# Kernel tuning notes

Hardware: AMD Instinct MI355X
Metric: run time of the kernel (lower is better)

The kernel has to match this reference:

```python
import jax, jax.numpy as jnp
import numpy as np

E = 1024
H = 16
D = E // H
S = 2048
B = 2

def setup_inputs() -> dict:
    key = jax.random.key(0)
    ks = jax.random.split(key, 5)
    x = jax.random.normal(ks[0], (B, S, E), dtype=jnp.float32)
    W_qkv = jax.random.normal(ks[1], (E, 3 * E), dtype=jnp.float32) / np.sqrt(E)
    b_qkv = jax.random.normal(ks[2], (3 * E,), dtype=jnp.float32) * 0.02
    W_out = jax.random.normal(ks[3], (E, E), dtype=jnp.float32) / np.sqrt(E)
    b_out = jax.random.normal(ks[4], (E,), dtype=jnp.float32) * 0.02
    return {"x": x, "W_qkv": W_qkv, "b_qkv": b_qkv, "W_out": W_out, "b_out": b_out}

def reference(x, W_qkv, b_qkv, W_out, b_out):
    b, s, e = x.shape
    qkv = x @ W_qkv + b_qkv                      # [B,S,3E]
    q, k, v = jnp.split(qkv, 3, axis=-1)
    # [B,S,E] -> [B,H,S,D]
    q = q.reshape(b, s, H, D).transpose(0, 2, 1, 3)
    k = k.reshape(b, s, H, D).transpose(0, 2, 1, 3)
    v = v.reshape(b, s, H, D).transpose(0, 2, 1, 3)
    scale = 1.0 / np.sqrt(D)
    att = jnp.einsum('bhqd,bhkd->bhqk', q, k) * scale
    causal = jnp.tril(jnp.ones((s, s), dtype=bool))
    att = jnp.where(causal[None, None], att, -jnp.inf)
    att = jax.nn.softmax(att, axis=-1)
    out = jnp.einsum('bhqk,bhkd->bhqd', att, v)  # [B,H,S,D]
    out = out.transpose(0, 2, 1, 3).reshape(b, s, e)
    return out @ W_out + b_out
```

## Files before the change

### kernel.cpp

```cpp
#include <hip/hip_runtime.h>

typedef unsigned short u16;
typedef __bf16  bf16x8 __attribute__((ext_vector_type(8)));
typedef float   f32x4  __attribute__((ext_vector_type(4)));
typedef unsigned int   u32x4 __attribute__((ext_vector_type(4)));
typedef unsigned short u16x4 __attribute__((ext_vector_type(4)));
typedef unsigned short u16x8 __attribute__((ext_vector_type(8)));

#define BB 2
#define HH 16
#define DD 64
#define SS 2048
#define EE 1024

#define QSCALE 0.1803368801111244f

static __device__ __forceinline__ u16 f2bf(float f) {
    unsigned int u = __float_as_uint(f);
    u += 0x7FFFu + ((u >> 16) & 1u);
    return (u16)(u >> 16);
}

union BfCast { u32x4 u; bf16x8 b; };
static __device__ __forceinline__ bf16x8 ldb8(const u16* p) {
    BfCast x; x.u = *(const u32x4*)p; return x.b;
}

static __device__ __forceinline__ void gload16(const u16* g, u16* l) {
    __builtin_amdgcn_global_load_lds(
        (const __attribute__((address_space(1))) unsigned int*)g,
        (__attribute__((address_space(3))) unsigned int*)l, 16, 0, 0);
}

#define UG (32 * 512)
static __device__ __forceinline__ int kidx(int s, int d) {
    return (((s >> 4) * 2 + (d >> 5)) * 512) + ((((d >> 3) & 3) * 16 + (s & 15)) * 8) + (d & 7);
}
static __device__ __forceinline__ int vidx(int key, int d) {
    return (((key >> 5) * 4 + (d >> 4)) * 512) + ((((key >> 3) & 3) * 16 + (d & 15)) * 8) + (key & 7);
}

__global__ __launch_bounds__(256) void prep_kernel(
    const float* __restrict__ x,    u16* __restrict__ xb,
    const float* __restrict__ Wqkv, u16* __restrict__ wqkvT,
    const float* __restrict__ Wout, u16* __restrict__ woutT)
{
    __shared__ float tile[32][33];
    const int bid = blockIdx.x;
    if (bid < 2048) {
        const int t = bid * 256 + threadIdx.x;
        const int u = t >> 6, w = t & 63;
        const int m = (u >> 5) * 16 + (w & 15);
        const int k = (u & 31) * 32 + (w >> 4) * 8;
        const float* p = x + m * 1024 + k;
        const f32x4 a = *(const f32x4*)p;
        const f32x4 b = *(const f32x4*)(p + 4);
        u16x8 o;
        o[0] = f2bf(a[0]); o[1] = f2bf(a[1]); o[2] = f2bf(a[2]); o[3] = f2bf(a[3]);
        o[4] = f2bf(b[0]); o[5] = f2bf(b[1]); o[6] = f2bf(b[2]); o[7] = f2bf(b[3]);
        *(u16x8*)&xb[u * 512 + w * 8] = o;
        return;
    }
    const float* in; u16* out; int C, tb;
    if (bid < 2048 + 3072) { in = Wqkv; out = wqkvT; C = 3072; tb = bid - 2048; }
    else                   { in = Wout; out = woutT; C = 1024; tb = bid - 5120; }
    const int tx = threadIdx.x & 31;
    const int ty = threadIdx.x >> 5;
    const int ct = C >> 5;
    const int bc = tb % ct, br = tb / ct;
    const int c0 = bc * 32, r0 = br * 32;
    #pragma unroll
    for (int i = 0; i < 4; i++)
        tile[ty + i * 8][tx] = in[(r0 + ty + i * 8) * C + c0 + tx];
    __syncthreads();
    #pragma unroll
    for (int i = 0; i < 4; i++) {
        const int n = c0 + ty + i * 8;
        out[((n >> 4) * 32 + (r0 >> 5)) * 512 + (((tx >> 3) & 3) * 16 + (n & 15)) * 8 + (tx & 7)]
            = f2bf(tile[tx][ty + i * 8]);
    }
}

__global__ __launch_bounds__(256, 3) void gemm_qkv_kernel(
    const u16* __restrict__ Af,
    const u16* __restrict__ Bf,
    const float* __restrict__ bias,
    u16* __restrict__ Qb, u16* __restrict__ Kb, u16* __restrict__ Vb)
{
    __shared__ __align__(16) u16 Bs[2][8 * 512];
    const int lane = threadIdx.x & 63;
    const int wave = threadIdx.x >> 6;
    const int nb = 3 * EE / 128;
    const int tm = blockIdx.x / nb, tn = blockIdx.x % nb;
    const int lm = lane & 15, quad = lane >> 4;
    const int wy = wave >> 1, wx = wave & 1;

    const u16* bg = Bf + (tn * 8 + 2 * wave) * UG + lane * 8;
    u16* bl0 = &Bs[0][2 * wave * 512];
    u16* bl1 = &Bs[1][2 * wave * 512];
    const u16* ag[4];
    #pragma unroll
    for (int i = 0; i < 4; i++)
        ag[i] = Af + (tm * 8 + wy * 4 + i) * UG + lane * 8;

    f32x4 acc[4][4] = {};
    bf16x8 a0[4], a1[4];

    gload16(bg,      bl0);
    gload16(bg + UG, bl0 + 512);
    #pragma unroll
    for (int i = 0; i < 4; i++) a0[i] = ldb8(ag[i]);

    #pragma unroll 1
    for (int it = 0; it < 32; it += 2) {
        __syncthreads();
        if (it + 1 < 32) {
            gload16(bg + (it + 1) * 512,      bl1);
            gload16(bg + UG + (it + 1) * 512, bl1 + 512);
            #pragma unroll
            for (int i = 0; i < 4; i++) a1[i] = ldb8(ag[i] + (it + 1) * 512);
        }
        {
            bf16x8 bf[4];
            #pragma unroll
            for (int i = 0; i < 4; i++)
                bf[i] = ldb8(&Bs[0][(wx * 4 + i) * 512 + lane * 8]);
            #pragma unroll
            for (int mi = 0; mi < 4; mi++)
                #pragma unroll
                for (int ni = 0; ni < 4; ni++)
                    acc[mi][ni] = __builtin_amdgcn_mfma_f32_16x16x32_bf16(a0[mi], bf[ni], acc[mi][ni], 0, 0, 0);
        }
        __syncthreads();
        if (it + 2 < 32) {
            gload16(bg + (it + 2) * 512,      bl0);
            gload16(bg + UG + (it + 2) * 512, bl0 + 512);
            #pragma unroll
            for (int i = 0; i < 4; i++) a0[i] = ldb8(ag[i] + (it + 2) * 512);
        }
        {
            bf16x8 bf[4];
            #pragma unroll
            for (int i = 0; i < 4; i++)
                bf[i] = ldb8(&Bs[1][(wx * 4 + i) * 512 + lane * 8]);
            #pragma unroll
            for (int mi = 0; mi < 4; mi++)
                #pragma unroll
                for (int ni = 0; ni < 4; ni++)
                    acc[mi][ni] = __builtin_amdgcn_mfma_f32_16x16x32_bf16(a1[mi], bf[ni], acc[mi][ni], 0, 0, 0);
        }
    }

    const int gm0 = tm * 128 + wy * 64;
    const int gn0 = tn * 128 + wx * 64;
    #pragma unroll
    for (int ni = 0; ni < 4; ni++) {
        const int n = gn0 + ni * 16 + lm;
        const float bv = bias[n];
        const int which = n >> 10;
        const int e = n & 1023;
        const int h = e >> 6, d = e & 63;
        #pragma unroll
        for (int mi = 0; mi < 4; mi++) {
            if (which == 2) {
                const int m0 = gm0 + mi * 16 + quad * 4;
                const int b = m0 >> 11, key0 = m0 & 2047;
                u16x4 pk;
                #pragma unroll
                for (int r = 0; r < 4; r++) pk[r] = f2bf(acc[mi][ni][r] + bv);
                *(u16x4*)&Vb[(b * HH + h) * 131072 + vidx(key0, d)] = pk;
            } else if (which == 1) {
                #pragma unroll
                for (int r = 0; r < 4; r++) {
                    const int m = gm0 + mi * 16 + quad * 4 + r;
                    const int b = m >> 11, s = m & 2047;
                    Kb[(b * HH + h) * 131072 + kidx(s, d)] = f2bf(acc[mi][ni][r] + bv);
                }
            } else {
                #pragma unroll
                for (int r = 0; r < 4; r++) {
                    const int m = gm0 + mi * 16 + quad * 4 + r;
                    const int b = m >> 11, s = m & 2047;
                    Qb[((b * HH + h) * SS + s) * DD + d] = f2bf((acc[mi][ni][r] + bv) * QSCALE);
                }
            }
        }
    }
}

__global__ __launch_bounds__(256) void attn_kernel(
    const u16* __restrict__ Qb, const u16* __restrict__ Kb,
    const u16* __restrict__ Vb, u16* __restrict__ Ob)
{
    __shared__ __align__(16) u16 Ks[2][4096];
    __shared__ __align__(16) u16 Vs[2][4096];
    __shared__ __align__(16) u16 Plds[4 * 16 * 72];
    const int tid = threadIdx.x;
    const int lane = tid & 63, wave = tid >> 6;
    const int lm = lane & 15, quad = lane >> 4;
    const int bh = blockIdx.x & 31;
    const int qt = (SS / 64 - 1) - (blockIdx.x >> 5);
    const int q0 = qt * 64;
    const int qrow = q0 + wave * 16;
    const int b = bh >> 4, h = bh & 15;

    const u16* qbase = Qb + (bh * SS + qrow) * DD;
    const bf16x8 qf0 = ldb8(qbase + lm * DD + quad * 8);
    const bf16x8 qf1 = ldb8(qbase + lm * DD + 32 + quad * 8);

    const u16* ktile = Kb + bh * 131072;
    const u16* vtile = Vb + bh * 131072;
    u16* Pw = Plds + wave * (16 * 72);

    BfCast oc; oc.u = (u32x4){0x3F803F80u, 0x3F803F80u, 0x3F803F80u, 0x3F803F80u};
    const bf16x8 ones = oc.b;

    f32x4 oacc[4] = {};
    f32x4 lacc = {0.f, 0.f, 0.f, 0.f};

    const int ktmax = qt + 1;
    {
        const u16* kg = ktile + wave * 1024 + lane * 8;
        const u16* vg = vtile + wave * 1024 + lane * 8;
        gload16(kg,       &Ks[0][wave * 1024]);
        gload16(kg + 512, &Ks[0][wave * 1024 + 512]);
        gload16(vg,       &Vs[0][wave * 1024]);
        gload16(vg + 512, &Vs[0][wave * 1024 + 512]);
    }
    for (int kt = 0; kt < ktmax; ++kt) {
        const int cur = kt & 1;
        const int k0 = kt * 64;
        __syncthreads();
        if (kt + 1 < ktmax) {
            const u16* kg = ktile + (kt + 1) * 4096 + wave * 1024 + lane * 8;
            const u16* vg = vtile + (kt + 1) * 4096 + wave * 1024 + lane * 8;
            gload16(kg,       &Ks[cur ^ 1][wave * 1024]);
            gload16(kg + 512, &Ks[cur ^ 1][wave * 1024 + 512]);
            gload16(vg,       &Vs[cur ^ 1][wave * 1024]);
            gload16(vg + 512, &Vs[cur ^ 1][wave * 1024 + 512]);
        }

        f32x4 s[4];
        #pragma unroll
        for (int g = 0; g < 4; g++) {
            f32x4 z = {0.f, 0.f, 0.f, 0.f};
            z    = __builtin_amdgcn_mfma_f32_16x16x32_bf16(ldb8(&Ks[cur][(g * 2) * 512 + lane * 8]), qf0, z, 0, 0, 0);
            s[g] = __builtin_amdgcn_mfma_f32_16x16x32_bf16(ldb8(&Ks[cur][(g * 2 + 1) * 512 + lane * 8]), qf1, z, 0, 0, 0);
        }
        if (k0 + 63 > qrow) {
            const int lim = qrow + lm - k0 - quad * 4;
            #pragma unroll
            for (int g = 0; g < 4; g++)
                #pragma unroll
                for (int r = 0; r < 4; r++)
                    if (g * 16 + r > lim) s[g][r] = -INFINITY;
        }
        #pragma unroll
        for (int g = 0; g < 4; g++) {
            u16x4 pk;
            #pragma unroll
            for (int r = 0; r < 4; r++) pk[r] = f2bf(__builtin_amdgcn_exp2f(s[g][r]));
            *(u16x4*)&Pw[lm * 72 + g * 16 + quad * 4] = pk;
        }
        const bf16x8 pf0 = ldb8(&Pw[lm * 72 + quad * 8]);
        const bf16x8 pf1 = ldb8(&Pw[lm * 72 + 32 + quad * 8]);
        lacc = __builtin_amdgcn_mfma_f32_16x16x32_bf16(ones, pf0, lacc, 0, 0, 0);
        lacc = __builtin_amdgcn_mfma_f32_16x16x32_bf16(ones, pf1, lacc, 0, 0, 0);
        #pragma unroll
        for (int dg = 0; dg < 4; dg++) {
            oacc[dg] = __builtin_amdgcn_mfma_f32_16x16x32_bf16(ldb8(&Vs[cur][dg * 512 + lane * 8]), pf0, oacc[dg], 0, 0, 0);
            oacc[dg] = __builtin_amdgcn_mfma_f32_16x16x32_bf16(ldb8(&Vs[cur][(4 + dg) * 512 + lane * 8]), pf1, oacc[dg], 0, 0, 0);
        }
    }
    const float inv = 1.0f / lacc[0];
    u16* ob = Ob + (((b * SS + qrow) >> 4) * 32 + h * 2) * 512;
    #pragma unroll
    for (int dg = 0; dg < 4; dg++) {
        u16x4 pk;
        #pragma unroll
        for (int r = 0; r < 4; r++) pk[r] = f2bf(oacc[dg][r] * inv);
        *(u16x4*)&ob[(dg >> 1) * 512 + (((dg * 2 + (quad >> 1)) & 3) * 16 + lm) * 8 + (quad & 1) * 4] = pk;
    }
}

__global__ __launch_bounds__(256) void gemm_out_kernel(
    const u16* __restrict__ Af,
    const u16* __restrict__ Bf,
    const float* __restrict__ bias,
    float* __restrict__ Out)
{
    __shared__ __align__(16) u16 Bs[2][8 * 512];
    const int lane = threadIdx.x & 63;
    const int wave = threadIdx.x >> 6;
    const int nb = EE / 128;
    const int tm = blockIdx.x / nb, tn = blockIdx.x % nb;
    const int lm = lane & 15, quad = lane >> 4;
    const int wy = wave >> 1, wx = wave & 1;

    const u16* bg = Bf + (tn * 8 + 2 * wave) * UG + lane * 8;
    u16* bl0 = &Bs[0][2 * wave * 512];
    u16* bl1 = &Bs[1][2 * wave * 512];
    const u16* ag[2];
    #pragma unroll
    for (int i = 0; i < 2; i++)
        ag[i] = Af + (tm * 4 + wy * 2 + i) * UG + lane * 8;

    f32x4 acc[2][4] = {};
    bf16x8 a0[2], a1[2];

    gload16(bg,      bl0);
    gload16(bg + UG, bl0 + 512);
    #pragma unroll
    for (int i = 0; i < 2; i++) a0[i] = ldb8(ag[i]);

    #pragma unroll 1
    for (int it = 0; it < 32; it += 2) {
        __syncthreads();
        if (it + 1 < 32) {
            gload16(bg + (it + 1) * 512,      bl1);
            gload16(bg + UG + (it + 1) * 512, bl1 + 512);
            #pragma unroll
            for (int i = 0; i < 2; i++) a1[i] = ldb8(ag[i] + (it + 1) * 512);
        }
        {
            bf16x8 bf[4];
            #pragma unroll
            for (int i = 0; i < 4; i++)
                bf[i] = ldb8(&Bs[0][(wx * 4 + i) * 512 + lane * 8]);
            #pragma unroll
            for (int mi = 0; mi < 2; mi++)
                #pragma unroll
                for (int ni = 0; ni < 4; ni++)
                    acc[mi][ni] = __builtin_amdgcn_mfma_f32_16x16x32_bf16(a0[mi], bf[ni], acc[mi][ni], 0, 0, 0);
        }
        __syncthreads();
        if (it + 2 < 32) {
            gload16(bg + (it + 2) * 512,      bl0);
            gload16(bg + UG + (it + 2) * 512, bl0 + 512);
            #pragma unroll
            for (int i = 0; i < 2; i++) a0[i] = ldb8(ag[i] + (it + 2) * 512);
        }
        {
            bf16x8 bf[4];
            #pragma unroll
            for (int i = 0; i < 4; i++)
                bf[i] = ldb8(&Bs[1][(wx * 4 + i) * 512 + lane * 8]);
            #pragma unroll
            for (int mi = 0; mi < 2; mi++)
                #pragma unroll
                for (int ni = 0; ni < 4; ni++)
                    acc[mi][ni] = __builtin_amdgcn_mfma_f32_16x16x32_bf16(a1[mi], bf[ni], acc[mi][ni], 0, 0, 0);
        }
    }

    const int gm0 = tm * 64 + wy * 32;
    const int gn0 = tn * 128 + wx * 64;
    #pragma unroll
    for (int ni = 0; ni < 4; ni++) {
        const int n = gn0 + ni * 16 + lm;
        const float bv = bias[n];
        #pragma unroll
        for (int mi = 0; mi < 2; mi++)
            #pragma unroll
            for (int r = 0; r < 4; r++)
                Out[(gm0 + mi * 16 + quad * 4 + r) * EE + n] = acc[mi][ni][r] + bv;
    }
}

extern "C" void kernel_launch(void* const* d_in, const int* in_sizes, int n_in,
                              void* d_out, int out_size, void* d_ws, size_t ws_size,
                              hipStream_t stream)
{
    const float* x     = (const float*)d_in[0];
    const float* Wqkv  = (const float*)d_in[1];
    const float* bqkv  = (const float*)d_in[2];
    const float* Wout  = (const float*)d_in[3];
    const float* bout  = (const float*)d_in[4];
    float* out = (float*)d_out;

    char* ws = (char*)d_ws;
    u16* xb    = (u16*)(ws + 0);
    u16* wqkvT = (u16*)(ws + 8388608);
    u16* woutT = (u16*)(ws + 14680064);
    u16* Qb    = (u16*)(ws + 16777216);
    u16* Kb    = (u16*)(ws + 25165824);
    u16* Vb    = (u16*)(ws + 33554432);
    u16* Ob    = (u16*)(ws + 41943040);
    if (ws_size < 50331648) return;

    prep_kernel<<<2048 + 3072 + 1024, 256, 0, stream>>>(x, xb, Wqkv, wqkvT, Wout, woutT);
    gemm_qkv_kernel<<<(BB * SS / 128) * (3 * EE / 128), 256, 0, stream>>>(xb, wqkvT, bqkv, Qb, Kb, Vb);
    attn_kernel<<<BB * HH * (SS / 64), 256, 0, stream>>>(Qb, Kb, Vb, Ob);
    gemm_out_kernel<<<(BB * SS / 64) * (EE / 128), 256, 0, stream>>>(Ob, woutT, bout, out);
}
```

Before: 174.8 us.

## Fuse all four stages into one persistent kernel with grid barriers

Replaces the four launches (prep, QKV GEMM, attention, output GEMM) with a single persistent kernel of 512 blocks. Stages are separated by atomic-counter grid barriers, and the GEMM and attention stages pull work items from atomic tile counters. The goal is to remove launch gaps and tail effects between kernels. In exchange it adds a hipMemsetAsync, spin-wait barriers that depend on all 512 blocks being co-resident (the spin has a guard that breaks out after a fixed count, which could let a block proceed before the others finish), and forces launch_bounds(256,3) on the attention stage.

```diff
diff --git a/kernel.cpp b/kernel.cpp
--- a/kernel.cpp
+++ b/kernel.cpp
@@ -40,15 +40,39 @@
     return (((key >> 5) * 4 + (d >> 4)) * 512) + ((((key >> 3) & 3) * 16 + (d & 15)) * 8) + (key & 7);
 }
 
-__global__ __launch_bounds__(256) void prep_kernel(
+static __device__ __forceinline__ void gbar(unsigned int* bar, unsigned int target) {
+    __syncthreads();
+    if (threadIdx.x == 0) {
+        __threadfence();
+        atomicAdd(bar, 1u);
+        unsigned int guard = 0;
+        while (atomicAdd(bar, 0u) < target) {
+            if (++guard > (1u << 22)) break;
+        }
+        __threadfence();
+    }
+    __syncthreads();
+}
+
+__global__ __launch_bounds__(256, 3) void fused_kernel(
     const float* __restrict__ x,    u16* __restrict__ xb,
     const float* __restrict__ Wqkv, u16* __restrict__ wqkvT,
-    const float* __restrict__ Wout, u16* __restrict__ woutT)
+    const float* __restrict__ Wout, u16* __restrict__ woutT,
+    const float* __restrict__ bqkv,
+    u16* __restrict__ Qb, u16* __restrict__ Kb, u16* __restrict__ Vb,
+    u16* __restrict__ Ob,
+    const float* __restrict__ bout, float* __restrict__ Out,
+    unsigned int* __restrict__ cnt)
 {
-    __shared__ float tile[32][33];
+    __shared__ __align__(16) u16 smem[21120];
+    __shared__ unsigned int su;
     const int bid = blockIdx.x;
-    if (bid < 2048) {
-        const int t = bid * 256 + threadIdx.x;
+    const int tid = threadIdx.x;
+    const int lane = tid & 63, wave = tid >> 6;
+    const int lm = lane & 15, quad = lane >> 4;
+
+    for (int cb = bid; cb < 2048; cb += 512) {
+        const int t = cb * 256 + tid;
         const int u = t >> 6, w = t & 63;
         const int m = (u >> 5) * 16 + (w & 15);
         const int k = (u & 31) * 32 + (w >> 4) * 8;
@@ -59,311 +83,307 @@
         o[0] = f2bf(a[0]); o[1] = f2bf(a[1]); o[2] = f2bf(a[2]); o[3] = f2bf(a[3]);
         o[4] = f2bf(b[0]); o[5] = f2bf(b[1]); o[6] = f2bf(b[2]); o[7] = f2bf(b[3]);
         *(u16x8*)&xb[u * 512 + w * 8] = o;
-        return;
-    }
-    const float* in; u16* out; int C, tb;
-    if (bid < 2048 + 3072) { in = Wqkv; out = wqkvT; C = 3072; tb = bid - 2048; }
-    else                   { in = Wout; out = woutT; C = 1024; tb = bid - 5120; }
-    const int tx = threadIdx.x & 31;
-    const int ty = threadIdx.x >> 5;
-    const int ct = C >> 5;
-    const int bc = tb % ct, br = tb / ct;
-    const int c0 = bc * 32, r0 = br * 32;
-    #pragma unroll
-    for (int i = 0; i < 4; i++)
-        tile[ty + i * 8][tx] = in[(r0 + ty + i * 8) * C + c0 + tx];
-    __syncthreads();
-    #pragma unroll
-    for (int i = 0; i < 4; i++) {
-        const int n = c0 + ty + i * 8;
-        out[((n >> 4) * 32 + (r0 >> 5)) * 512 + (((tx >> 3) & 3) * 16 + (n & 15)) * 8 + (tx & 7)]
-            = f2bf(tile[tx][ty + i * 8]);
-    }
-}
-
-__global__ __launch_bounds__(256, 3) void gemm_qkv_kernel(
-    const u16* __restrict__ Af,
-    const u16* __restrict__ Bf,
-    const float* __restrict__ bias,
-    u16* __restrict__ Qb, u16* __restrict__ Kb, u16* __restrict__ Vb)
-{
-    __shared__ __align__(16) u16 Bs[2][8 * 512];
-    const int lane = threadIdx.x & 63;
-    const int wave = threadIdx.x >> 6;
-    const int nb = 3 * EE / 128;
-    const int tm = blockIdx.x / nb, tn = blockIdx.x % nb;
-    const int lm = lane & 15, quad = lane >> 4;
-    const int wy = wave >> 1, wx = wave & 1;
-
-    const u16* bg = Bf + (tn * 8 + 2 * wave) * UG + lane * 8;
-    u16* bl0 = &Bs[0][2 * wave * 512];
-    u16* bl1 = &Bs[1][2 * wave * 512];
-    const u16* ag[4];
-    #pragma unroll
-    for (int i = 0; i < 4; i++)
-        ag[i] = Af + (tm * 8 + wy * 4 + i) * UG + lane * 8;
-
-    f32x4 acc[4][4] = {};
-    bf16x8 a0[4], a1[4];
-
-    gload16(bg,      bl0);
-    gload16(bg + UG, bl0 + 512);
-    #pragma unroll
-    for (int i = 0; i < 4; i++) a0[i] = ldb8(ag[i]);
-
-    #pragma unroll 1
-    for (int it = 0; it < 32; it += 2) {
-        __syncthreads();
-        if (it + 1 < 32) {
-            gload16(bg + (it + 1) * 512,      bl1);
-            gload16(bg + UG + (it + 1) * 512, bl1 + 512);
-            #pragma unroll
-            for (int i = 0; i < 4; i++) a1[i] = ldb8(ag[i] + (it + 1) * 512);
-        }
-        {
-            bf16x8 bf[4];
+    }
+    {
+        float* tile = (float*)smem;
+        const int tx = tid & 31, ty = tid >> 5;
+        for (int tb = bid; tb < 4096; tb += 512) {
+            const float* in; u16* out; int C, b2;
+            if (tb < 3072) { in = Wqkv; out = wqkvT; C = 3072; b2 = tb; }
+            else           { in = Wout; out = woutT; C = 1024; b2 = tb - 3072; }
+            const int ct = C >> 5;
+            const int bc = b2 % ct, br = b2 / ct;
+            const int c0 = bc * 32, r0 = br * 32;
+            __syncthreads();
             #pragma unroll
             for (int i = 0; i < 4; i++)
-                bf[i] = ldb8(&Bs[0][(wx * 4 + i) * 512 + lane * 8]);
+                tile[(ty + i * 8) * 33 + tx] = in[(r0 + ty + i * 8) * C + c0 + tx];
+            __syncthreads();
             #pragma unroll
-            for (int mi = 0; mi < 4; mi++)
-                #pragma unroll
-                for (int ni = 0; ni < 4; ni++)
-                    acc[mi][ni] = __builtin_amdgcn_mfma_f32_16x16x32_bf16(a0[mi], bf[ni], acc[mi][ni], 0, 0, 0);
-        }
-        __syncthreads();
-        if (it + 2 < 32) {
-            gload16(bg + (it + 2) * 512,      bl0);
-            gload16(bg + UG + (it + 2) * 512, bl0 + 512);
+            for (int i = 0; i < 4; i++) {
+                const int n = c0 + ty + i * 8;
+                out[((n >> 4) * 32 + (r0 >> 5)) * 512 + (((tx >> 3) & 3) * 16 + (n & 15)) * 8 + (tx & 7)]
+                    = f2bf(tile[tx * 33 + ty + i * 8]);
+            }
+        }
+    }
+    gbar(cnt, 512);
+
+    {
+        const int wy = wave >> 1, wx = wave & 1;
+        for (;;) {
+            __syncthreads();
+            if (tid == 0) su = atomicAdd(cnt + 16, 1u);
+            __syncthreads();
+            const int uq = (int)su;
+            if (uq >= 768) break;
+            const int tm = uq / 24, tn = uq % 24;
+
+            const u16* bg = wqkvT + (tn * 8 + 2 * wave) * UG + lane * 8;
+            u16* bl0 = smem + 2 * wave * 512;
+            u16* bl1 = smem + 4096 + 2 * wave * 512;
+            const u16* ag0 = xb + (tm * 8 + wy * 4 + 0) * UG + lane * 8;
+            const u16* ag1 = xb + (tm * 8 + wy * 4 + 1) * UG + lane * 8;
+            const u16* ag2 = xb + (tm * 8 + wy * 4 + 2) * UG + lane * 8;
+            const u16* ag3 = xb + (tm * 8 + wy * 4 + 3) * UG + lane * 8;
+
+            f32x4 acc[4][4] = {};
+            bf16x8 a0[4], a1[4];
+
+            gload16(bg,      bl0);
+            gload16(bg + UG, bl0 + 512);
+            a0[0] = ldb8(ag0); a0[1] = ldb8(ag1); a0[2] = ldb8(ag2); a0[3] = ldb8(ag3);
+
+            #pragma unroll 1
+            for (int it = 0; it < 32; it += 2) {
+                __syncthreads();
+                if (it + 1 < 32) {
+                    gload16(bg + (it + 1) * 512,      bl1);
+                    gload16(bg + UG + (it + 1) * 512, bl1 + 512);
+                    a1[0] = ldb8(ag0 + (it + 1) * 512);
+                    a1[1] = ldb8(ag1 + (it + 1) * 512);
+                    a1[2] = ldb8(ag2 + (it + 1) * 512);
+                    a1[3] = ldb8(ag3 + (it + 1) * 512);
+                }
+                {
+                    bf16x8 bf[4];
+                    #pragma unroll
+                    for (int i = 0; i < 4; i++)
+                        bf[i] = ldb8(smem + (wx * 4 + i) * 512 + lane * 8);
+                    #pragma unroll
+                    for (int mi = 0; mi < 4; mi++)
+                        #pragma unroll
+                        for (int ni = 0; ni < 4; ni++)
+                            acc[mi][ni] = __builtin_amdgcn_mfma_f32_16x16x32_bf16(a0[mi], bf[ni], acc[mi][ni], 0, 0, 0);
+                }
+                __syncthreads();
+                if (it + 2 < 32) {
+                    gload16(bg + (it + 2) * 512,      bl0);
+                    gload16(bg + UG + (it + 2) * 512, bl0 + 512);
+                    a0[0] = ldb8(ag0 + (it + 2) * 512);
+                    a0[1] = ldb8(ag1 + (it + 2) * 512);
+                    a0[2] = ldb8(ag2 + (it + 2) * 512);
+                    a0[3] = ldb8(ag3 + (it + 2) * 512);
+                }
+                {
+                    bf16x8 bf[4];
+                    #pragma unroll
+                    for (int i = 0; i < 4; i++)
+                        bf[i] = ldb8(smem + 4096 + (wx * 4 + i) * 512 + lane * 8);
+                    #pragma unroll
+                    for (int mi = 0; mi < 4; mi++)
+                        #pragma unroll
+                        for (int ni = 0; ni < 4; ni++)
+                            acc[mi][ni] = __builtin_amdgcn_mfma_f32_16x16x32_bf16(a1[mi], bf[ni], acc[mi][ni], 0, 0, 0);
+                }
+            }
+
+            const int gm0 = tm * 128 + wy * 64;
+            const int gn0 = tn * 128 + wx * 64;
             #pragma unroll
-            for (int i = 0; i < 4; i++) a0[i] = ldb8(ag[i] + (it + 2) * 512);
-        }
-        {
-            bf16x8 bf[4];
+            for (int ni = 0; ni < 4; ni++) {
+                const int n = gn0 + ni * 16 + lm;
+                const float bv = bqkv[n];
+                const int which = n >> 10;
+                const int e = n & 1023;
+                const int h = e >> 6, d = e & 63;
+                #pragma unroll
+                for (int mi = 0; mi < 4; mi++) {
+                    if (which == 2) {
+                        const int m0 = gm0 + mi * 16 + quad * 4;
+                        const int b = m0 >> 11, key0 = m0 & 2047;
+                        u16x4 pk;
+                        #pragma unroll
+                        for (int r = 0; r < 4; r++) pk[r] = f2bf(acc[mi][ni][r] + bv);
+                        *(u16x4*)&Vb[(b * HH + h) * 131072 + vidx(key0, d)] = pk;
+                    } else if (which == 1) {
+                        #pragma unroll
+                        for (int r = 0; r < 4; r++) {
+                            const int m = gm0 + mi * 16 + quad * 4 + r;
+                            const int b = m >> 11, s = m & 2047;
+                            Kb[(b * HH + h) * 131072 + kidx(s, d)] = f2bf(acc[mi][ni][r] + bv);
+                        }
+                    } else {
+                        #pragma unroll
+                        for (int r = 0; r < 4; r++) {
+                            const int m = gm0 + mi * 16 + quad * 4 + r;
+                            const int b = m >> 11, s = m & 2047;
+                            Qb[((b * HH + h) * SS + s) * DD + d] = f2bf((acc[mi][ni][r] + bv) * QSCALE);
+                        }
+                    }
+                }
+            }
+        }
+    }
+    gbar(cnt, 1024);
+
+    {
+        u16* Pw = smem + 16384 + wave * (16 * 72);
+        BfCast oc; oc.u = (u32x4){0x3F803F80u, 0x3F803F80u, 0x3F803F80u, 0x3F803F80u};
+        const bf16x8 ones = oc.b;
+
+        for (;;) {
+            __syncthreads();
+            if (tid == 0) su = atomicAdd(cnt + 32, 1u);
+            __syncthreads();
+            const int u = (int)su;
+            if (u >= 1024) break;
+            const int bh = u & 31;
+            const int qt = (SS / 64 - 1) - (u >> 5);
+            const int q0 = qt * 64;
+            const int qrow = q0 + wave * 16;
+            const int b = bh >> 4, h = bh & 15;
+
+            const u16* qbase = Qb + (bh * SS + qrow) * DD;
+            const bf16x8 qf0 = ldb8(qbase + lm * DD + quad * 8);
+            const bf16x8 qf1 = ldb8(qbase + lm * DD + 32 + quad * 8);
+
+            const u16* ktile = Kb + bh * 131072;
+            const u16* vtile = Vb + bh * 131072;
+
+            f32x4 oacc[4] = {};
+            f32x4 lacc = {0.f, 0.f, 0.f, 0.f};
+
+            const int ktmax = qt + 1;
+            {
+                const u16* kg = ktile + wave * 1024 + lane * 8;
+                const u16* vg = vtile + wave * 1024 + lane * 8;
+                gload16(kg,       smem + wave * 1024);
+                gload16(kg + 512, smem + wave * 1024 + 512);
+                gload16(vg,       smem + 8192 + wave * 1024);
+                gload16(vg + 512, smem + 8192 + wave * 1024 + 512);
+            }
+            for (int kt = 0; kt < ktmax; ++kt) {
+                const int cur = kt & 1;
+                const int k0 = kt * 64;
+                u16* Kcur = smem + cur * 4096;
+                u16* Vcur = smem + 8192 + cur * 4096;
+                __syncthreads();
+                if (kt + 1 < ktmax) {
+                    u16* Knxt = smem + (cur ^ 1) * 4096;
+                    u16* Vnxt = smem + 8192 + (cur ^ 1) * 4096;
+                    const u16* kg = ktile + (kt + 1) * 4096 + wave * 1024 + lane * 8;
+                    const u16* vg = vtile + (kt + 1) * 4096 + wave * 1024 + lane * 8;
+                    gload16(kg,       Knxt + wave * 1024);
+                    gload16(kg + 512, Knxt + wave * 1024 + 512);
+                    gload16(vg,       Vnxt + wave * 1024);
+                    gload16(vg + 512, Vnxt + wave * 1024 + 512);
+                }
+
+                f32x4 s[4];
+                #pragma unroll
+                for (int g = 0; g < 4; g++) {
+                    f32x4 z = {0.f, 0.f, 0.f, 0.f};
+                    z    = __builtin_amdgcn_mfma_f32_16x16x32_bf16(ldb8(Kcur + (g * 2) * 512 + lane * 8), qf0, z, 0, 0, 0);
+                    s[g] = __builtin_amdgcn_mfma_f32_16x16x32_bf16(ldb8(Kcur + (g * 2 + 1) * 512 + lane * 8), qf1, z, 0, 0, 0);
+                }
+                if (k0 + 63 > qrow) {
+                    const int lim = qrow + lm - k0 - quad * 4;
+                    #pragma unroll
+                    for (int g = 0; g < 4; g++)
+                        #pragma unroll
+                        for (int r = 0; r < 4; r++)
+                            if (g * 16 + r > lim) s[g][r] = -INFINITY;
+                }
+                #pragma unroll
+                for (int g = 0; g < 4; g++) {
+                    u16x4 pk;
+                    #pragma unroll
+                    for (int r = 0; r < 4; r++) pk[r] = f2bf(__builtin_amdgcn_exp2f(s[g][r]));
+                    *(u16x4*)&Pw[lm * 72 + g * 16 + quad * 4] = pk;
+                }
+                const bf16x8 pf0 = ldb8(&Pw[lm * 72 + quad * 8]);
+                const bf16x8 pf1 = ldb8(&Pw[lm * 72 + 32 + quad * 8]);
+                lacc = __builtin_amdgcn_mfma_f32_16x16x32_bf16(ones, pf0, lacc, 0, 0, 0);
+                lacc = __builtin_amdgcn_mfma_f32_16x16x32_bf16(ones, pf1, lacc, 0, 0, 0);
+                #pragma unroll
+                for (int dg = 0; dg < 4; dg++) {
+                    oacc[dg] = __builtin_amdgcn_mfma_f32_16x16x32_bf16(ldb8(Vcur + dg * 512 + lane * 8), pf0, oacc[dg], 0, 0, 0);
+                    oacc[dg] = __builtin_amdgcn_mfma_f32_16x16x32_bf16(ldb8(Vcur + (4 + dg) * 512 + lane * 8), pf1, oacc[dg], 0, 0, 0);
+                }
+            }
+            const float inv = 1.0f / lacc[0];
+            u16* ob = Ob + (((b * SS + qrow) >> 4) * 32 + h * 2) * 512;
             #pragma unroll
-            for (int i = 0; i < 4; i++)
-                bf[i] = ldb8(&Bs[1][(wx * 4 + i) * 512 + lane * 8]);
-            #pragma unroll
-            for (int mi = 0; mi < 4; mi++)
-                #pragma unroll
-                for (int ni = 0; ni < 4; ni++)
-                    acc[mi][ni] = __builtin_amdgcn_mfma_f32_16x16x32_bf16(a1[mi], bf[ni], acc[mi][ni], 0, 0, 0);
-        }
-    }
-
-    const int gm0 = tm * 128 + wy * 64;
-    const int gn0 = tn * 128 + wx * 64;
-    #pragma unroll
-    for (int ni = 0; ni < 4; ni++) {
-        const int n = gn0 + ni * 16 + lm;
-        const float bv = bias[n];
-        const int which = n >> 10;
-        const int e = n & 1023;
-        const int h = e >> 6, d = e & 63;
+            for (int dg = 0; dg < 4; dg++) {
+                u16x4 pk;
+                #pragma unroll
+                for (int r = 0; r < 4; r++) pk[r] = f2bf(oacc[dg][r] * inv);
+                *(u16x4*)&ob[(dg >> 1) * 512 + (((dg * 2 + (quad >> 1)) & 3) * 16 + lm) * 8 + (quad & 1) * 4] = pk;
+            }
+        }
+    }
+    gbar(cnt, 1536);
+
+    {
+        const int tm = bid / 8, tn = bid % 8;
+        const int wy = wave >> 1, wx = wave & 1;
+
+        const u16* bg = woutT + (tn * 8 + 2 * wave) * UG + lane * 8;
+        u16* bl0 = smem + 2 * wave * 512;
+        u16* bl1 = smem + 4096 + 2 * wave * 512;
+        const u16* ag0 = Ob + (tm * 4 + wy * 2 + 0) * UG + lane * 8;
+        const u16* ag1 = Ob + (tm * 4 + wy * 2 + 1) * UG + lane * 8;
+
+        f32x4 acc[2][4] = {};
+        bf16x8 a0[2], a1[2];
+
+        gload16(bg,      bl0);
+        gload16(bg + UG, bl0 + 512);
+        a0[0] = ldb8(ag0); a0[1] = ldb8(ag1);
+
+        #pragma unroll 1
+        for (int it = 0; it < 32; it += 2) {
+            __syncthreads();
+            if (it + 1 < 32) {
+                gload16(bg + (it + 1) * 512,      bl1);
+                gload16(bg + UG + (it + 1) * 512, bl1 + 512);
+                a1[0] = ldb8(ag0 + (it + 1) * 512);
+                a1[1] = ldb8(ag1 + (it + 1) * 512);
+            }
+            {
+                bf16x8 bf[4];
+                #pragma unroll
+                for (int i = 0; i < 4; i++)
+                    bf[i] = ldb8(smem + (wx * 4 + i) * 512 + lane * 8);
+                #pragma unroll
+                for (int mi = 0; mi < 2; mi++)
+                    #pragma unroll
+                    for (int ni = 0; ni < 4; ni++)
+                        acc[mi][ni] = __builtin_amdgcn_mfma_f32_16x16x32_bf16(a0[mi], bf[ni], acc[mi][ni], 0, 0, 0);
+            }
+            __syncthreads();
+            if (it + 2 < 32) {
+                gload16(bg + (it + 2) * 512,      bl0);
+                gload16(bg + UG + (it + 2) * 512, bl0 + 512);
+                a0[0] = ldb8(ag0 + (it + 2) * 512);
+                a0[1] = ldb8(ag1 + (it + 2) * 512);
+            }
+            {
+                bf16x8 bf[4];
+                #pragma unroll
+                for (int i = 0; i < 4; i++)
+                    bf[i] = ldb8(smem + 4096 + (wx * 4 + i) * 512 + lane * 8);
+                #pragma unroll
+                for (int mi = 0; mi < 2; mi++)
+                    #pragma unroll
+                    for (int ni = 0; ni < 4; ni++)
+                        acc[mi][ni] = __builtin_amdgcn_mfma_f32_16x16x32_bf16(a1[mi], bf[ni], acc[mi][ni], 0, 0, 0);
+            }
+        }
+
+        const int gm0 = tm * 64 + wy * 32;
+        const int gn0 = tn * 128 + wx * 64;
         #pragma unroll
-        for (int mi = 0; mi < 4; mi++) {
-            if (which == 2) {
-                const int m0 = gm0 + mi * 16 + quad * 4;
-                const int b = m0 >> 11, key0 = m0 & 2047;
-                u16x4 pk;
-                #pragma unroll
-                for (int r = 0; r < 4; r++) pk[r] = f2bf(acc[mi][ni][r] + bv);
-                *(u16x4*)&Vb[(b * HH + h) * 131072 + vidx(key0, d)] = pk;
-            } else if (which == 1) {
-                #pragma unroll
-                for (int r = 0; r < 4; r++) {
-                    const int m = gm0 + mi * 16 + quad * 4 + r;
-                    const int b = m >> 11, s = m & 2047;
-                    Kb[(b * HH + h) * 131072 + kidx(s, d)] = f2bf(acc[mi][ni][r] + bv);
-                }
-            } else {
-                #pragma unroll
-                for (int r = 0; r < 4; r++) {
-                    const int m = gm0 + mi * 16 + quad * 4 + r;
-                    const int b = m >> 11, s = m & 2047;
-                    Qb[((b * HH + h) * SS + s) * DD + d] = f2bf((acc[mi][ni][r] + bv) * QSCALE);
-                }
-            }
-        }
-    }
-}
-
-__global__ __launch_bounds__(256) void attn_kernel(
-    const u16* __restrict__ Qb, const u16* __restrict__ Kb,
-    const u16* __restrict__ Vb, u16* __restrict__ Ob)
-{
-    __shared__ __align__(16) u16 Ks[2][4096];
-    __shared__ __align__(16) u16 Vs[2][4096];
-    __shared__ __align__(16) u16 Plds[4 * 16 * 72];
-    const int tid = threadIdx.x;
-    const int lane = tid & 63, wave = tid >> 6;
-    const int lm = lane & 15, quad = lane >> 4;
-    const int bh = blockIdx.x & 31;
-    const int qt = (SS / 64 - 1) - (blockIdx.x >> 5);
-    const int q0 = qt * 64;
-    const int qrow = q0 + wave * 16;
-    const int b = bh >> 4, h = bh & 15;
-
-    const u16* qbase = Qb + (bh * SS + qrow) * DD;
-    const bf16x8 qf0 = ldb8(qbase + lm * DD + quad * 8);
-    const bf16x8 qf1 = ldb8(qbase + lm * DD + 32 + quad * 8);
-
-    const u16* ktile = Kb + bh * 131072;
-    const u16* vtile = Vb + bh * 131072;
-    u16* Pw = Plds + wave * (16 * 72);
-
-    BfCast oc; oc.u = (u32x4){0x3F803F80u, 0x3F803F80u, 0x3F803F80u, 0x3F803F80u};
-    const bf16x8 ones = oc.b;
-
-    f32x4 oacc[4] = {};
-    f32x4 lacc = {0.f, 0.f, 0.f, 0.f};
-
-    const int ktmax = qt + 1;
-    {
-        const u16* kg = ktile + wave * 1024 + lane * 8;
-        const u16* vg = vtile + wave * 1024 + lane * 8;
-        gload16(kg,       &Ks[0][wave * 1024]);
-        gload16(kg + 512, &Ks[0][wave * 1024 + 512]);
-        gload16(vg,       &Vs[0][wave * 1024]);
-        gload16(vg + 512, &Vs[0][wave * 1024 + 512]);
-    }
-    for (int kt = 0; kt < ktmax; ++kt) {
-        const int cur = kt & 1;
-        const int k0 = kt * 64;
-        __syncthreads();
-        if (kt + 1 < ktmax) {
-            const u16* kg = ktile + (kt + 1) * 4096 + wave * 1024 + lane * 8;
-            const u16* vg = vtile + (kt + 1) * 4096 + wave * 1024 + lane * 8;
-            gload16(kg,       &Ks[cur ^ 1][wave * 1024]);
-            gload16(kg + 512, &Ks[cur ^ 1][wave * 1024 + 512]);
-            gload16(vg,       &Vs[cur ^ 1][wave * 1024]);
-            gload16(vg + 512, &Vs[cur ^ 1][wave * 1024 + 512]);
-        }
-
-        f32x4 s[4];
-        #pragma unroll
-        for (int g = 0; g < 4; g++) {
-            f32x4 z = {0.f, 0.f, 0.f, 0.f};
-            z    = __builtin_amdgcn_mfma_f32_16x16x32_bf16(ldb8(&Ks[cur][(g * 2) * 512 + lane * 8]), qf0, z, 0, 0, 0);
-            s[g] = __builtin_amdgcn_mfma_f32_16x16x32_bf16(ldb8(&Ks[cur][(g * 2 + 1) * 512 + lane * 8]), qf1, z, 0, 0, 0);
-        }
-        if (k0 + 63 > qrow) {
-            const int lim = qrow + lm - k0 - quad * 4;
-            #pragma unroll
-            for (int g = 0; g < 4; g++)
-                #pragma unroll
-                for (int r = 0; r < 4; r++)
-                    if (g * 16 + r > lim) s[g][r] = -INFINITY;
-        }
-        #pragma unroll
-        for (int g = 0; g < 4; g++) {
-            u16x4 pk;
-            #pragma unroll
-            for (int r = 0; r < 4; r++) pk[r] = f2bf(__builtin_amdgcn_exp2f(s[g][r]));
-            *(u16x4*)&Pw[lm * 72 + g * 16 + quad * 4] = pk;
-        }
-        const bf16x8 pf0 = ldb8(&Pw[lm * 72 + quad * 8]);
-        const bf16x8 pf1 = ldb8(&Pw[lm * 72 + 32 + quad * 8]);
-        lacc = __builtin_amdgcn_mfma_f32_16x16x32_bf16(ones, pf0, lacc, 0, 0, 0);
-        lacc = __builtin_amdgcn_mfma_f32_16x16x32_bf16(ones, pf1, lacc, 0, 0, 0);
-        #pragma unroll
-        for (int dg = 0; dg < 4; dg++) {
-            oacc[dg] = __builtin_amdgcn_mfma_f32_16x16x32_bf16(ldb8(&Vs[cur][dg * 512 + lane * 8]), pf0, oacc[dg], 0, 0, 0);
-            oacc[dg] = __builtin_amdgcn_mfma_f32_16x16x32_bf16(ldb8(&Vs[cur][(4 + dg) * 512 + lane * 8]), pf1, oacc[dg], 0, 0, 0);
-        }
-    }
-    const float inv = 1.0f / lacc[0];
-    u16* ob = Ob + (((b * SS + qrow) >> 4) * 32 + h * 2) * 512;
-    #pragma unroll
-    for (int dg = 0; dg < 4; dg++) {
-        u16x4 pk;
-        #pragma unroll
-        for (int r = 0; r < 4; r++) pk[r] = f2bf(oacc[dg][r] * inv);
-        *(u16x4*)&ob[(dg >> 1) * 512 + (((dg * 2 + (quad >> 1)) & 3) * 16 + lm) * 8 + (quad & 1) * 4] = pk;
-    }
-}
-
-__global__ __launch_bounds__(256) void gemm_out_kernel(
-    const u16* __restrict__ Af,
-    const u16* __restrict__ Bf,
-    const float* __restrict__ bias,
-    float* __restrict__ Out)
-{
-    __shared__ __align__(16) u16 Bs[2][8 * 512];
-    const int lane = threadIdx.x & 63;
-    const int wave = threadIdx.x >> 6;
-    const int nb = EE / 128;
-    const int tm = blockIdx.x / nb, tn = blockIdx.x % nb;
-    const int lm = lane & 15, quad = lane >> 4;
-    const int wy = wave >> 1, wx = wave & 1;
-
-    const u16* bg = Bf + (tn * 8 + 2 * wave) * UG + lane * 8;
-    u16* bl0 = &Bs[0][2 * wave * 512];
-    u16* bl1 = &Bs[1][2 * wave * 512];
-    const u16* ag[2];
-    #pragma unroll
-    for (int i = 0; i < 2; i++)
-        ag[i] = Af + (tm * 4 + wy * 2 + i) * UG + lane * 8;
-
-    f32x4 acc[2][4] = {};
-    bf16x8 a0[2], a1[2];
-
-    gload16(bg,      bl0);
-    gload16(bg + UG, bl0 + 512);
-    #pragma unroll
-    for (int i = 0; i < 2; i++) a0[i] = ldb8(ag[i]);
-
-    #pragma unroll 1
-    for (int it = 0; it < 32; it += 2) {
-        __syncthreads();
-        if (it + 1 < 32) {
-            gload16(bg + (it + 1) * 512,      bl1);
-            gload16(bg + UG + (it + 1) * 512, bl1 + 512);
-            #pragma unroll
-            for (int i = 0; i < 2; i++) a1[i] = ldb8(ag[i] + (it + 1) * 512);
-        }
-        {
-            bf16x8 bf[4];
-            #pragma unroll
-            for (int i = 0; i < 4; i++)
-                bf[i] = ldb8(&Bs[0][(wx * 4 + i) * 512 + lane * 8]);
+        for (int ni = 0; ni < 4; ni++) {
+            const int n = gn0 + ni * 16 + lm;
+            const float bv = bout[n];
             #pragma unroll
             for (int mi = 0; mi < 2; mi++)
                 #pragma unroll
-                for (int ni = 0; ni < 4; ni++)
-                    acc[mi][ni] = __builtin_amdgcn_mfma_f32_16x16x32_bf16(a0[mi], bf[ni], acc[mi][ni], 0, 0, 0);
-        }
-        __syncthreads();
-        if (it + 2 < 32) {
-            gload16(bg + (it + 2) * 512,      bl0);
-            gload16(bg + UG + (it + 2) * 512, bl0 + 512);
-            #pragma unroll
-            for (int i = 0; i < 2; i++) a0[i] = ldb8(ag[i] + (it + 2) * 512);
-        }
-        {
-            bf16x8 bf[4];
-            #pragma unroll
-            for (int i = 0; i < 4; i++)
-                bf[i] = ldb8(&Bs[1][(wx * 4 + i) * 512 + lane * 8]);
-            #pragma unroll
-            for (int mi = 0; mi < 2; mi++)
-                #pragma unroll
-                for (int ni = 0; ni < 4; ni++)
-                    acc[mi][ni] = __builtin_amdgcn_mfma_f32_16x16x32_bf16(a1[mi], bf[ni], acc[mi][ni], 0, 0, 0);
-        }
-    }
-
-    const int gm0 = tm * 64 + wy * 32;
-    const int gn0 = tn * 128 + wx * 64;
-    #pragma unroll
-    for (int ni = 0; ni < 4; ni++) {
-        const int n = gn0 + ni * 16 + lm;
-        const float bv = bias[n];
-        #pragma unroll
-        for (int mi = 0; mi < 2; mi++)
-            #pragma unroll
-            for (int r = 0; r < 4; r++)
-                Out[(gm0 + mi * 16 + quad * 4 + r) * EE + n] = acc[mi][ni][r] + bv;
+                for (int r = 0; r < 4; r++)
+                    Out[(gm0 + mi * 16 + quad * 4 + r) * EE + n] = acc[mi][ni][r] + bv;
+        }
     }
 }
 
@@ -386,10 +406,10 @@
     u16* Kb    = (u16*)(ws + 25165824);
     u16* Vb    = (u16*)(ws + 33554432);
     u16* Ob    = (u16*)(ws + 41943040);
-    if (ws_size < 50331648) return;
-
-    prep_kernel<<<2048 + 3072 + 1024, 256, 0, stream>>>(x, xb, Wqkv, wqkvT, Wout, woutT);
-    gemm_qkv_kernel<<<(BB * SS / 128) * (3 * EE / 128), 256, 0, stream>>>(xb, wqkvT, bqkv, Qb, Kb, Vb);
-    attn_kernel<<<BB * HH * (SS / 64), 256, 0, stream>>>(Qb, Kb, Vb, Ob);
-    gemm_out_kernel<<<(BB * SS / 64) * (EE / 128), 256, 0, stream>>>(Ob, woutT, bout, out);
-}
+    unsigned int* cnt = (unsigned int*)(ws + 50331648);
+    if (ws_size < 50331648 + 4096) return;
+
+    (void)hipMemsetAsync(cnt, 0, 256, stream);
+    fused_kernel<<<512, 256, 0, stream>>>(x, xb, Wqkv, wqkvT, Wout, woutT, bqkv,
+                                          Qb, Kb, Vb, Ob, bout, out, cnt);
+}
```

New measurement: 392.0 us. 124% more time.

## Load GEMM B fragments directly from global memory into registers, dropping LDS staging

Applied to the files above, without the earlier changes.

Both the QKV and output-projection GEMM kernels now load their pre-swizzled B fragments straight from global memory into registers, with double-buffered register prefetch. The shared-memory buffers and the two __syncthreads per iteration are gone. This removes LDS traffic and barrier stalls, but each wave now fetches its B tile independently, so global/L2 reads of B double (two wy waves share each wx column) and register pressure rises.

```diff
diff --git a/kernel.cpp b/kernel.cpp
--- a/kernel.cpp
+++ b/kernel.cpp
@@ -87,7 +87,6 @@
     const float* __restrict__ bias,
     u16* __restrict__ Qb, u16* __restrict__ Kb, u16* __restrict__ Vb)
 {
-    __shared__ __align__(16) u16 Bs[2][8 * 512];
     const int lane = threadIdx.x & 63;
     const int wave = threadIdx.x >> 6;
     const int nb = 3 * EE / 128;
@@ -95,60 +94,47 @@
     const int lm = lane & 15, quad = lane >> 4;
     const int wy = wave >> 1, wx = wave & 1;
 
-    const u16* bg = Bf + (tn * 8 + 2 * wave) * UG + lane * 8;
-    u16* bl0 = &Bs[0][2 * wave * 512];
-    u16* bl1 = &Bs[1][2 * wave * 512];
-    const u16* ag[4];
-    #pragma unroll
-    for (int i = 0; i < 4; i++)
-        ag[i] = Af + (tm * 8 + wy * 4 + i) * UG + lane * 8;
+    const u16* ag0 = Af + (tm * 8 + wy * 4 + 0) * UG + lane * 8;
+    const u16* ag1 = Af + (tm * 8 + wy * 4 + 1) * UG + lane * 8;
+    const u16* ag2 = Af + (tm * 8 + wy * 4 + 2) * UG + lane * 8;
+    const u16* ag3 = Af + (tm * 8 + wy * 4 + 3) * UG + lane * 8;
+    const u16* bg0 = Bf + (tn * 8 + wx * 4 + 0) * UG + lane * 8;
+    const u16* bg1 = Bf + (tn * 8 + wx * 4 + 1) * UG + lane * 8;
+    const u16* bg2 = Bf + (tn * 8 + wx * 4 + 2) * UG + lane * 8;
+    const u16* bg3 = Bf + (tn * 8 + wx * 4 + 3) * UG + lane * 8;
 
     f32x4 acc[4][4] = {};
-    bf16x8 a0[4], a1[4];
-
-    gload16(bg,      bl0);
-    gload16(bg + UG, bl0 + 512);
-    #pragma unroll
-    for (int i = 0; i < 4; i++) a0[i] = ldb8(ag[i]);
+    bf16x8 a0[4], b0[4], a1[4], b1[4];
+
+    a0[0] = ldb8(ag0); a0[1] = ldb8(ag1); a0[2] = ldb8(ag2); a0[3] = ldb8(ag3);
+    b0[0] = ldb8(bg0); b0[1] = ldb8(bg1); b0[2] = ldb8(bg2); b0[3] = ldb8(bg3);
 
     #pragma unroll 1
     for (int it = 0; it < 32; it += 2) {
-        __syncthreads();
+        const int k1 = (it + 1) * 512;
         if (it + 1 < 32) {
-            gload16(bg + (it + 1) * 512,      bl1);
-            gload16(bg + UG + (it + 1) * 512, bl1 + 512);
-            #pragma unroll
-            for (int i = 0; i < 4; i++) a1[i] = ldb8(ag[i] + (it + 1) * 512);
-        }
-        {
-            bf16x8 bf[4];
-            #pragma unroll
-            for (int i = 0; i < 4; i++)
-                bf[i] = ldb8(&Bs[0][(wx * 4 + i) * 512 + lane * 8]);
-            #pragma unroll
-            for (int mi = 0; mi < 4; mi++)
-                #pragma unroll
-                for (int ni = 0; ni < 4; ni++)
-                    acc[mi][ni] = __builtin_amdgcn_mfma_f32_16x16x32_bf16(a0[mi], bf[ni], acc[mi][ni], 0, 0, 0);
-        }
-        __syncthreads();
+            a1[0] = ldb8(ag0 + k1); a1[1] = ldb8(ag1 + k1);
+            a1[2] = ldb8(ag2 + k1); a1[3] = ldb8(ag3 + k1);
+            b1[0] = ldb8(bg0 + k1); b1[1] = ldb8(bg1 + k1);
+            b1[2] = ldb8(bg2 + k1); b1[3] = ldb8(bg3 + k1);
+        }
+        #pragma unroll
+        for (int mi = 0; mi < 4; mi++)
+            #pragma unroll
+            for (int ni = 0; ni < 4; ni++)
+                acc[mi][ni] = __builtin_amdgcn_mfma_f32_16x16x32_bf16(a0[mi], b0[ni], acc[mi][ni], 0, 0, 0);
+        const int k2 = (it + 2) * 512;
         if (it + 2 < 32) {
-            gload16(bg + (it + 2) * 512,      bl0);
-            gload16(bg + UG + (it + 2) * 512, bl0 + 512);
-            #pragma unroll
-            for (int i = 0; i < 4; i++) a0[i] = ldb8(ag[i] + (it + 2) * 512);
-        }
-        {
-            bf16x8 bf[4];
-            #pragma unroll
-            for (int i = 0; i < 4; i++)
-                bf[i] = ldb8(&Bs[1][(wx * 4 + i) * 512 + lane * 8]);
-            #pragma unroll
-            for (int mi = 0; mi < 4; mi++)
-                #pragma unroll
-                for (int ni = 0; ni < 4; ni++)
-                    acc[mi][ni] = __builtin_amdgcn_mfma_f32_16x16x32_bf16(a1[mi], bf[ni], acc[mi][ni], 0, 0, 0);
-        }
+            a0[0] = ldb8(ag0 + k2); a0[1] = ldb8(ag1 + k2);
+            a0[2] = ldb8(ag2 + k2); a0[3] = ldb8(ag3 + k2);
+            b0[0] = ldb8(bg0 + k2); b0[1] = ldb8(bg1 + k2);
+            b0[2] = ldb8(bg2 + k2); b0[3] = ldb8(bg3 + k2);
+        }
+        #pragma unroll
+        for (int mi = 0; mi < 4; mi++)
+            #pragma unroll
+            for (int ni = 0; ni < 4; ni++)
+                acc[mi][ni] = __builtin_amdgcn_mfma_f32_16x16x32_bf16(a1[mi], b1[ni], acc[mi][ni], 0, 0, 0);
     }
 
     const int gm0 = tm * 128 + wy * 64;
@@ -289,7 +275,6 @@
     const float* __restrict__ bias,
     float* __restrict__ Out)
 {
-    __shared__ __align__(16) u16 Bs[2][8 * 512];
     const int lane = threadIdx.x & 63;
     const int wave = threadIdx.x >> 6;
     const int nb = EE / 128;
@@ -297,60 +282,43 @@
     const int lm = lane & 15, quad = lane >> 4;
     const int wy = wave >> 1, wx = wave & 1;
 
-    const u16* bg = Bf + (tn * 8 + 2 * wave) * UG + lane * 8;
-    u16* bl0 = &Bs[0][2 * wave * 512];
-    u16* bl1 = &Bs[1][2 * wave * 512];
-    const u16* ag[2];
-    #pragma unroll
-    for (int i = 0; i < 2; i++)
-        ag[i] = Af + (tm * 4 + wy * 2 + i) * UG + lane * 8;
+    const u16* ag0 = Af + (tm * 4 + wy * 2 + 0) * UG + lane * 8;
+    const u16* ag1 = Af + (tm * 4 + wy * 2 + 1) * UG + lane * 8;
+    const u16* bg0 = Bf + (tn * 8 + wx * 4 + 0) * UG + lane * 8;
+    const u16* bg1 = Bf + (tn * 8 + wx * 4 + 1) * UG + lane * 8;
+    const u16* bg2 = Bf + (tn * 8 + wx * 4 + 2) * UG + lane * 8;
+    const u16* bg3 = Bf + (tn * 8 + wx * 4 + 3) * UG + lane * 8;
 
     f32x4 acc[2][4] = {};
-    bf16x8 a0[2], a1[2];
-
-    gload16(bg,      bl0);
-    gload16(bg + UG, bl0 + 512);
-    #pragma unroll
-    for (int i = 0; i < 2; i++) a0[i] = ldb8(ag[i]);
+    bf16x8 a0[2], b0[4], a1[2], b1[4];
+
+    a0[0] = ldb8(ag0); a0[1] = ldb8(ag1);
+    b0[0] = ldb8(bg0); b0[1] = ldb8(bg1); b0[2] = ldb8(bg2); b0[3] = ldb8(bg3);
 
     #pragma unroll 1
     for (int it = 0; it < 32; it += 2) {
-        __syncthreads();
+        const int k1 = (it + 1) * 512;
         if (it + 1 < 32) {
-            gload16(bg + (it + 1) * 512,      bl1);
-            gload16(bg + UG + (it + 1) * 512, bl1 + 512);
-            #pragma unroll
-            for (int i = 0; i < 2; i++) a1[i] = ldb8(ag[i] + (it + 1) * 512);
-        }
-        {
-            bf16x8 bf[4];
-            #pragma unroll
-            for (int i = 0; i < 4; i++)
-                bf[i] = ldb8(&Bs[0][(wx * 4 + i) * 512 + lane * 8]);
-            #pragma unroll
-            for (int mi = 0; mi < 2; mi++)
-                #pragma unroll
-                for (int ni = 0; ni < 4; ni++)
-                    acc[mi][ni] = __builtin_amdgcn_mfma_f32_16x16x32_bf16(a0[mi], bf[ni], acc[mi][ni], 0, 0, 0);
-        }
-        __syncthreads();
+            a1[0] = ldb8(ag0 + k1); a1[1] = ldb8(ag1 + k1);
+            b1[0] = ldb8(bg0 + k1); b1[1] = ldb8(bg1 + k1);
+            b1[2] = ldb8(bg2 + k1); b1[3] = ldb8(bg3 + k1);
+        }
+        #pragma unroll
+        for (int mi = 0; mi < 2; mi++)
+            #pragma unroll
+            for (int ni = 0; ni < 4; ni++)
+                acc[mi][ni] = __builtin_amdgcn_mfma_f32_16x16x32_bf16(a0[mi], b0[ni], acc[mi][ni], 0, 0, 0);
+        const int k2 = (it + 2) * 512;
         if (it + 2 < 32) {
-            gload16(bg + (it + 2) * 512,      bl0);
-            gload16(bg + UG + (it + 2) * 512, bl0 + 512);
-            #pragma unroll
-            for (int i = 0; i < 2; i++) a0[i] = ldb8(ag[i] + (it + 2) * 512);
-        }
-        {
-            bf16x8 bf[4];
-            #pragma unroll
-            for (int i = 0; i < 4; i++)
-                bf[i] = ldb8(&Bs[1][(wx * 4 + i) * 512 + lane * 8]);
-            #pragma unroll
-            for (int mi = 0; mi < 2; mi++)
-                #pragma unroll
-                for (int ni = 0; ni < 4; ni++)
-                    acc[mi][ni] = __builtin_amdgcn_mfma_f32_16x16x32_bf16(a1[mi], bf[ni], acc[mi][ni], 0, 0, 0);
-        }
+            a0[0] = ldb8(ag0 + k2); a0[1] = ldb8(ag1 + k2);
+            b0[0] = ldb8(bg0 + k2); b0[1] = ldb8(bg1 + k2);
+            b0[2] = ldb8(bg2 + k2); b0[3] = ldb8(bg3 + k2);
+        }
+        #pragma unroll
+        for (int mi = 0; mi < 2; mi++)
+            #pragma unroll
+            for (int ni = 0; ni < 4; ni++)
+                acc[mi][ni] = __builtin_amdgcn_mfma_f32_16x16x32_bf16(a1[mi], b1[ni], acc[mi][ni], 0, 0, 0);
     }
 
     const int gm0 = tm * 64 + wy * 32;
```

Result: no change. 174.2 us (-0.4%).
